# Optimization experiments

Hardware: AMD Instinct MI355X
Metric: run time of the kernel (lower is better)

The kernel has to match this reference:

```python
import jax, jax.numpy as jnp
import numpy as np

# static config (matches init_kwargs / input_specs)
LENS = (2048, 1024, 512, 256)   # per-level temporal lengths, sum = 3840
N, LQ, D_MODEL = 8, 2048, 256
M, L, P = 8, 4, 4               # heads, levels, points
D_HEAD = D_MODEL // M           # 32


def setup_inputs() -> dict:
    key = jax.random.key(0)
    ks = jax.random.split(key, 8)
    s = 0.02  # xavier-ish scale for 256-wide linears
    return {
        "query": jax.random.normal(ks[0], (N, LQ, D_MODEL), jnp.float32),
        "reference_points": jax.random.uniform(ks[1], (N, LQ, L, 1), dtype=jnp.float32),
        "input_flatten": jax.random.normal(ks[2], (N, sum(LENS), D_MODEL), jnp.float32),
        "input_temporal_lens": jnp.array(LENS, jnp.int32),
        "input_level_start_index": jnp.array(np.concatenate([[0], np.cumsum(LENS)[:-1]]), jnp.int32),
        "W_val": jax.random.normal(ks[3], (D_MODEL, D_MODEL), jnp.float32) * s,
        "b_val": jnp.zeros((D_MODEL,), jnp.float32),
        "W_off": jax.random.normal(ks[4], (M * L * P, D_MODEL), jnp.float32) * s,
        "b_off": jax.random.normal(ks[5], (M * L * P,), jnp.float32),  # mimics linspace bias init
        "W_attn": jax.random.normal(ks[6], (M * L * P, D_MODEL), jnp.float32) * s,
        "b_attn": jnp.zeros((M * L * P,), jnp.float32),
    }


def _sample_level(v, x, T):
    """1D bilinear sampling with zero padding, matching F.grid_sample
    (mode='bilinear', padding_mode='zeros', align_corners=False) on a (1,T) map.
    v: (N, T, M, D) level values; x: (N, Lq, M, P) normalized locations in [0,1].
    Returns (N, Lq, M, P, D)."""
    n, lq, m, p = x.shape
    ix = x * T - 0.5
    ix0 = jnp.floor(ix)
    w1 = (ix - ix0)[..., None]            # (N,Lq,M,P,1)
    i0 = ix0.astype(jnp.int32)

    def gather(idx):
        valid = ((idx >= 0) & (idx < T)).astype(v.dtype)
        idxc = jnp.clip(idx, 0, T - 1)
        flat = idxc.transpose(0, 1, 3, 2).reshape(n, lq * p, m)       # (N, Lq*P, M)
        g = jnp.take_along_axis(v, flat[..., None], axis=1)           # (N, Lq*P, M, D)
        g = g * valid.transpose(0, 1, 3, 2).reshape(n, lq * p, m)[..., None]
        return g.reshape(n, lq, p, m, -1).transpose(0, 1, 3, 2, 4)    # (N,Lq,M,P,D)

    return gather(i0) * (1.0 - w1) + gather(i0 + 1) * w1


def _deform_core(value, lens, loc, attn):
    """value: (N, S, M, D); loc: (N,Lq,M,L,P,1); attn: (N,Lq,M,L,P) -> (N,Lq,M*D)"""
    out = 0.0
    start = 0
    for lid, T in enumerate(lens):
        v = value[:, start:start + T]
        start += T
        s = _sample_level(v, loc[:, :, :, lid, :, 0], T)              # (N,Lq,M,P,D)
        out = out + jnp.einsum('nqmpd,nqmp->nqmd', s, attn[:, :, :, lid])
    n, lq, m, d = out.shape
    return out.reshape(n, lq, m * d)


def reference(query, reference_points, input_flatten, input_temporal_lens,
              input_level_start_index, W_val, b_val, W_off, b_off, W_attn, b_attn):
    lens = LENS  # static per-level lengths (needed for static slicing)
    value = (input_flatten @ W_val.T + b_val).reshape(N, sum(lens), M, D_HEAD)
    offs = (query @ W_off.T + b_off).reshape(N, LQ, M, L, P, 1)
    attn = jax.nn.softmax((query @ W_attn.T + b_attn).reshape(N, LQ, M, L * P), axis=-1)
    attn = attn.reshape(N, LQ, M, L, P)
    # reference_points last dim == 1, offset_normalizer=None branch
    norm = jnp.asarray(lens, query.dtype)[None, None, None, :, None, None]
    loc = reference_points[:, :, None, :, None, :] + offs / norm      # (N,Lq,M,L,P,1)
    # fp32 path of the torch module returns the core output WITHOUT output_proj
    return _deform_core(value, lens, loc, attn)
```

## Files before the change

kernel.cpp:

```cpp
#include <hip/hip_runtime.h>
#include <cstddef>

namespace {

constexpr int NB    = 8;
constexpr int LQn   = 2048;
constexpr int DM    = 256;
constexpr int S_TOT = 3840;

typedef __attribute__((ext_vector_type(8))) short  short8;
typedef __attribute__((ext_vector_type(4))) float  f32x4;
typedef __attribute__((ext_vector_type(8))) _Float16 half8;
typedef __attribute__((ext_vector_type(2))) _Float16 half2v;

__device__ inline unsigned short f2bf(float f) {
  union { float f; unsigned u; } v; v.f = f;
  const unsigned u = v.u;
  return (unsigned short)((u + 0x7FFFu + ((u >> 16) & 1u)) >> 16);
}

__global__ __launch_bounds__(256) void gemm_bf16_k(
    const float* __restrict__ A,
    const float* __restrict__ Wa, const float* __restrict__ ba,
    const float* __restrict__ Wb, const float* __restrict__ bb,
    _Float16* __restrict__ out)
{
  __shared__ short As[128 * 64];
  __shared__ short Bs[128 * 64];

  const int tid  = threadIdx.x;
  const int lane = tid & 63;
  const int wid  = tid >> 6;
  const int wm   = wid >> 1;
  const int wn   = wid & 1;
  const int r0   = blockIdx.x * 128;
  const int c0   = blockIdx.y * 128;

  const float* W    = Wa;
  const float* bias = ba;
  int cw0 = c0;
  if (Wb != nullptr && c0 >= 128) { W = Wb; bias = bb; cw0 = c0 - 128; }

  f32x4 acc[4][4] = {};

  float bv[4];
  #pragma unroll
  for (int ni = 0; ni < 4; ++ni)
    bv[ni] = bias[cw0 + wn * 64 + ni * 16 + (lane & 15)];

  f32x4 pa0[4], pa1[4], pw0[4], pw1[4];

  auto load_tiles = [&](int k0) {
    #pragma unroll
    for (int i = 0; i < 4; ++i) {
      const int ch  = tid + i * 256;
      const int row = ch >> 3;
      const int kg  = ch & 7;
      const size_t goff = (size_t)(r0 + row) * DM + k0 + kg * 8;
      pa0[i] = *reinterpret_cast<const f32x4*>(&A[goff]);
      pa1[i] = *reinterpret_cast<const f32x4*>(&A[goff + 4]);
      const size_t woff = (size_t)(cw0 + row) * DM + k0 + kg * 8;
      pw0[i] = *reinterpret_cast<const f32x4*>(&W[woff]);
      pw1[i] = *reinterpret_cast<const f32x4*>(&W[woff + 4]);
    }
  };

  load_tiles(0);

  for (int k = 0; k < 4; ++k) {
    #pragma unroll
    for (int i = 0; i < 4; ++i) {
      const int ch  = tid + i * 256;
      const int row = ch >> 3;
      const int kg  = ch & 7;
      short8 sa, sw;
      #pragma unroll
      for (int j = 0; j < 4; ++j) {
        sa[j]     = (short)f2bf(pa0[i][j]);
        sa[j + 4] = (short)f2bf(pa1[i][j]);
        sw[j]     = (short)f2bf(pw0[i][j]);
        sw[j + 4] = (short)f2bf(pw1[i][j]);
      }
      const int byte = row * 128 + ((kg * 16) ^ ((row & 7) << 4));
      *reinterpret_cast<short8*>(reinterpret_cast<char*>(As) + byte) = sa;
      *reinterpret_cast<short8*>(reinterpret_cast<char*>(Bs) + byte) = sw;
    }
    if (k < 3) load_tiles((k + 1) * 64);

    asm volatile("s_waitcnt lgkmcnt(0)" ::: "memory");
    __builtin_amdgcn_sched_barrier(0);
    __builtin_amdgcn_s_barrier();
    __builtin_amdgcn_sched_barrier(0);

    #pragma unroll
    for (int ks = 0; ks < 2; ++ks) {
      const int kb = (ks * 32 + (lane >> 4) * 8) * 2;
      short8 af[4], bf[4];
      #pragma unroll
      for (int mi = 0; mi < 4; ++mi) {
        const int row = wm * 64 + mi * 16 + (lane & 15);
        const int byte = row * 128 + (kb ^ ((row & 7) << 4));
        af[mi] = *reinterpret_cast<const short8*>(
            reinterpret_cast<const char*>(As) + byte);
      }
      #pragma unroll
      for (int ni = 0; ni < 4; ++ni) {
        const int col = wn * 64 + ni * 16 + (lane & 15);
        const int byte = col * 128 + (kb ^ ((col & 7) << 4));
        bf[ni] = *reinterpret_cast<const short8*>(
            reinterpret_cast<const char*>(Bs) + byte);
      }
      #pragma unroll
      for (int mi = 0; mi < 4; ++mi)
        #pragma unroll
        for (int ni = 0; ni < 4; ++ni)
          acc[mi][ni] = __builtin_amdgcn_mfma_f32_16x16x32_bf16(
              af[mi], bf[ni], acc[mi][ni], 0, 0, 0);
    }

    asm volatile("s_waitcnt lgkmcnt(0)" ::: "memory");
    __builtin_amdgcn_sched_barrier(0);
    __builtin_amdgcn_s_barrier();
    __builtin_amdgcn_sched_barrier(0);
  }

  #pragma unroll
  for (int mi = 0; mi < 4; ++mi) {
    const int row = r0 + wm * 64 + mi * 16 + (lane >> 4) * 4;
    #pragma unroll
    for (int ni = 0; ni < 4; ++ni) {
      const int col = c0 + wn * 64 + ni * 16 + (lane & 15);
      #pragma unroll
      for (int j = 0; j < 4; ++j)
        out[(size_t)(row + j) * DM + col] = (_Float16)(acc[mi][ni][j] + bv[ni]);
    }
  }
}

__global__ __launch_bounds__(256) void sample_k(
    const _Float16* __restrict__ proj,
    const float* __restrict__ refp,
    const _Float16* __restrict__ value,
    float* __restrict__ out)
{
  constexpr int QPB = 8;
  __shared__ _Float16 proj_s[QPB][256];
  __shared__ float    ref_s[QPB][4];
  __shared__ uint4    tap_s[QPB][8 * 17];

  const int d     = blockIdx.x;
  const int n     = d & 7;
  const int chunk = d >> 3;
  const int row0q = n * LQn + chunk * QPB;
  const int t     = threadIdx.x;

  reinterpret_cast<half8*>(&proj_s[0][0])[t] =
      reinterpret_cast<const half8*>(proj + (size_t)row0q * DM)[t];
  if (t < QPB * 4)
    reinterpret_cast<float*>(ref_s)[t] = refp[(size_t)row0q * 4 + t];
  __syncthreads();

  const int   lens[4]   = {2048, 1024, 512, 256};
  const int   starts[4] = {0, 2048, 3072, 3584};

  {
    const int q   = t >> 5;
    const int m   = (t >> 2) & 7;
    const int sub = t & 3;
    const int j0  = m * 16 + sub * 4;

    float lg[4], off[4];
    #pragma unroll
    for (int i = 0; i < 4; ++i) {
      lg[i]  = (float)proj_s[q][128 + j0 + i];
      off[i] = (float)proj_s[q][j0 + i];
    }
    float mx = fmaxf(fmaxf(lg[0], lg[1]), fmaxf(lg[2], lg[3]));
    mx = fmaxf(mx, __shfl_xor(mx, 1));
    mx = fmaxf(mx, __shfl_xor(mx, 2));
    float e[4], s = 0.f;
    #pragma unroll
    for (int i = 0; i < 4; ++i) { e[i] = __expf(lg[i] - mx); s += e[i]; }
    s += __shfl_xor(s, 1);
    s += __shfl_xor(s, 2);
    const float inv = 1.f / s;

    const int   T  = lens[sub];
    const int   st = starts[sub];
    const float fT = (float)T;
    const float rf = ref_s[q][sub];
    #pragma unroll
    for (int i = 0; i < 4; ++i) {
      const float a  = e[i] * inv;
      const float ix = fmaf(rf, fT, off[i] - 0.5f);
      const float fl = floorf(ix);
      const float w1 = ix - fl;
      const int   i0 = (int)fl;
      const int   i1 = i0 + 1;
      const float wa = (i0 >= 0 && i0 < T) ? a * (1.f - w1) : 0.f;
      const float wb = (i1 >= 0 && i1 < T) ? a * w1 : 0.f;
      const int   r0b = (st + min(max(i0, 0), T - 1)) * 512;
      const int   r1b = (st + min(max(i1, 0), T - 1)) * 512;
      union { half2v h; unsigned u; } pw;
      pw.h.x = (_Float16)wa; pw.h.y = (_Float16)wb;
      uint4 ent; ent.x = pw.u; ent.y = (unsigned)r0b; ent.z = (unsigned)r1b; ent.w = 0u;
      tap_s[q][m * 17 + sub * 4 + i] = ent;
    }
  }
  __syncthreads();

  const int q  = t >> 5;
  const int m  = (t >> 2) & 7;
  const int dg = t & 3;
  const char* vb = reinterpret_cast<const char*>(value) +
                   (size_t)n * S_TOT * 512 + m * 64 + dg * 16;

  float acc[8] = {};
  #pragma unroll
  for (int tap = 0; tap < 16; ++tap) {
    const uint4 e = tap_s[q][m * 17 + tap];
    union { unsigned u; half2v h; } pw; pw.u = e.x;
    const float wa = (float)pw.h.x;
    const float wb = (float)pw.h.y;
    const half8 v0 = *reinterpret_cast<const half8*>(vb + e.y);
    const half8 v1 = *reinterpret_cast<const half8*>(vb + e.z);
    #pragma unroll
    for (int j = 0; j < 8; ++j)
      acc[j] = fmaf(wa, (float)v0[j], fmaf(wb, (float)v1[j], acc[j]));
  }

  float* op = &out[(size_t)(row0q + q) * DM + m * 32 + dg * 8];
  f32x4 o0 = {acc[0], acc[1], acc[2], acc[3]};
  f32x4 o1 = {acc[4], acc[5], acc[6], acc[7]};
  *reinterpret_cast<f32x4*>(op)     = o0;
  *reinterpret_cast<f32x4*>(op + 4) = o1;
}

}

extern "C" void kernel_launch(void* const* d_in, const int* in_sizes, int n_in,
                              void* d_out, int out_size, void* d_ws, size_t ws_size,
                              hipStream_t stream) {
  const float* query  = (const float*)d_in[0];
  const float* refp   = (const float*)d_in[1];
  const float* inflat = (const float*)d_in[2];
  const float* W_val  = (const float*)d_in[5];
  const float* b_val  = (const float*)d_in[6];
  const float* W_off  = (const float*)d_in[7];
  const float* b_off  = (const float*)d_in[8];
  const float* W_attn = (const float*)d_in[9];
  const float* b_attn = (const float*)d_in[10];
  float* out = (float*)d_out;

  _Float16* value_h = (_Float16*)d_ws;
  _Float16* proj_h  = (_Float16*)((char*)d_ws +
                      (size_t)NB * S_TOT * DM * sizeof(_Float16));

  dim3 blk(256);

  gemm_bf16_k<<<dim3((NB * S_TOT) / 128, DM / 128), blk, 0, stream>>>(
      inflat, W_val, b_val, nullptr, nullptr, value_h);

  gemm_bf16_k<<<dim3((NB * LQn) / 128, DM / 128), blk, 0, stream>>>(
      query, W_off, b_off, W_attn, b_attn, proj_h);

  sample_k<<<dim3(NB * LQn / 8), blk, 0, stream>>>(proj_h, refp, value_h, out);
}
```

Before: 46.67 us.

## Merge both projection GEMMs into one launch and split sampling taps across threads

The value and query projection GEMMs now run as one grid of 736 blocks, with each block picking its operands from its block index. This removes a launch and lets the two GEMMs fill the GPU together. The sampling kernel now uses 512 threads, and each (query, head, dgroup) is split across two threads that each handle 8 of the 16 taps, combined with a shuffle. This doubles the memory-level parallelism for the gathers. The shared-memory staging of proj and refp is dropped in favour of direct loads, which cuts one barrier but adds redundant global reads.

```diff
diff --git a/kernel.cpp b/kernel.cpp
--- a/kernel.cpp
+++ b/kernel.cpp
@@ -11,6 +11,7 @@
 typedef __attribute__((ext_vector_type(8))) short  short8;
 typedef __attribute__((ext_vector_type(4))) float  f32x4;
 typedef __attribute__((ext_vector_type(8))) _Float16 half8;
+typedef __attribute__((ext_vector_type(4))) _Float16 half4;
 typedef __attribute__((ext_vector_type(2))) _Float16 half2v;
 
 __device__ inline unsigned short f2bf(float f) {
@@ -20,10 +21,11 @@
 }
 
 __global__ __launch_bounds__(256) void gemm_bf16_k(
-    const float* __restrict__ A,
-    const float* __restrict__ Wa, const float* __restrict__ ba,
-    const float* __restrict__ Wb, const float* __restrict__ bb,
-    _Float16* __restrict__ out)
+    const float* __restrict__ A_val, const float* __restrict__ A_prj,
+    const float* __restrict__ W_val, const float* __restrict__ b_val,
+    const float* __restrict__ W_off, const float* __restrict__ b_off,
+    const float* __restrict__ W_att, const float* __restrict__ b_att,
+    _Float16* __restrict__ out_val, _Float16* __restrict__ out_prj)
 {
   __shared__ short As[128 * 64];
   __shared__ short Bs[128 * 64];
@@ -33,20 +35,27 @@
   const int wid  = tid >> 6;
   const int wm   = wid >> 1;
   const int wn   = wid & 1;
-  const int r0   = blockIdx.x * 128;
-  const int c0   = blockIdx.y * 128;
-
-  const float* W    = Wa;
-  const float* bias = ba;
-  int cw0 = c0;
-  if (Wb != nullptr && c0 >= 128) { W = Wb; bias = bb; cw0 = c0 - 128; }
+
+  const int id = blockIdx.x;
+  const float *A, *W, *bias;
+  _Float16* out;
+  int r0, c0;
+  if (id < 480) {
+    const int rb = id >> 1, c = id & 1;
+    A = A_val; out = out_val; r0 = rb * 128; c0 = c * 128;
+    W = W_val + (size_t)c0 * DM; bias = b_val + c0;
+  } else {
+    const int j = id - 480, rb = j >> 1, c = j & 1;
+    A = A_prj; out = out_prj; r0 = rb * 128; c0 = c * 128;
+    W = c ? W_att : W_off; bias = c ? b_att : b_off;
+  }
 
   f32x4 acc[4][4] = {};
 
   float bv[4];
   #pragma unroll
   for (int ni = 0; ni < 4; ++ni)
-    bv[ni] = bias[cw0 + wn * 64 + ni * 16 + (lane & 15)];
+    bv[ni] = bias[wn * 64 + ni * 16 + (lane & 15)];
 
   f32x4 pa0[4], pa1[4], pw0[4], pw1[4];
 
@@ -59,7 +68,7 @@
       const size_t goff = (size_t)(r0 + row) * DM + k0 + kg * 8;
       pa0[i] = *reinterpret_cast<const f32x4*>(&A[goff]);
       pa1[i] = *reinterpret_cast<const f32x4*>(&A[goff + 4]);
-      const size_t woff = (size_t)(cw0 + row) * DM + k0 + kg * 8;
+      const size_t woff = (size_t)row * DM + k0 + kg * 8;
       pw0[i] = *reinterpret_cast<const f32x4*>(&W[woff]);
       pw1[i] = *reinterpret_cast<const f32x4*>(&W[woff + 4]);
     }
@@ -137,44 +146,36 @@
   }
 }
 
-__global__ __launch_bounds__(256) void sample_k(
+__global__ __launch_bounds__(512) void sample_k(
     const _Float16* __restrict__ proj,
     const float* __restrict__ refp,
     const _Float16* __restrict__ value,
     float* __restrict__ out)
 {
-  constexpr int QPB = 8;
-  __shared__ _Float16 proj_s[QPB][256];
-  __shared__ float    ref_s[QPB][4];
-  __shared__ uint4    tap_s[QPB][8 * 17];
+  __shared__ uint4 tap_s[8][136];
 
   const int d     = blockIdx.x;
   const int n     = d & 7;
   const int chunk = d >> 3;
-  const int row0q = n * LQn + chunk * QPB;
+  const int row0q = n * LQn + chunk * 8;
   const int t     = threadIdx.x;
 
-  reinterpret_cast<half8*>(&proj_s[0][0])[t] =
-      reinterpret_cast<const half8*>(proj + (size_t)row0q * DM)[t];
-  if (t < QPB * 4)
-    reinterpret_cast<float*>(ref_s)[t] = refp[(size_t)row0q * 4 + t];
-  __syncthreads();
-
-  const int   lens[4]   = {2048, 1024, 512, 256};
-  const int   starts[4] = {0, 2048, 3072, 3584};
-
-  {
+  const int lens[4]   = {2048, 1024, 512, 256};
+  const int starts[4] = {0, 2048, 3072, 3584};
+
+  if (t < 256) {
     const int q   = t >> 5;
     const int m   = (t >> 2) & 7;
     const int sub = t & 3;
     const int j0  = m * 16 + sub * 4;
-
+    const size_t prow = (size_t)(row0q + q) * DM;
+
+    const half4 offv = *reinterpret_cast<const half4*>(&proj[prow + j0]);
+    const half4 lgv  = *reinterpret_cast<const half4*>(&proj[prow + 128 + j0]);
     float lg[4], off[4];
     #pragma unroll
-    for (int i = 0; i < 4; ++i) {
-      lg[i]  = (float)proj_s[q][128 + j0 + i];
-      off[i] = (float)proj_s[q][j0 + i];
-    }
+    for (int i = 0; i < 4; ++i) { lg[i] = (float)lgv[i]; off[i] = (float)offv[i]; }
+
     float mx = fmaxf(fmaxf(lg[0], lg[1]), fmaxf(lg[2], lg[3]));
     mx = fmaxf(mx, __shfl_xor(mx, 1));
     mx = fmaxf(mx, __shfl_xor(mx, 2));
@@ -188,7 +189,7 @@
     const int   T  = lens[sub];
     const int   st = starts[sub];
     const float fT = (float)T;
-    const float rf = ref_s[q][sub];
+    const float rf = refp[(size_t)(row0q + q) * 4 + sub];
     #pragma unroll
     for (int i = 0; i < 4; ++i) {
       const float a  = e[i] * inv;
@@ -209,16 +210,18 @@
   }
   __syncthreads();
 
-  const int q  = t >> 5;
-  const int m  = (t >> 2) & 7;
-  const int dg = t & 3;
+  const int q  = t >> 6;
+  const int l  = t & 63;
+  const int m  = l >> 3;
+  const int dg = l & 3;
+  const int th = (l >> 2) & 1;
   const char* vb = reinterpret_cast<const char*>(value) +
                    (size_t)n * S_TOT * 512 + m * 64 + dg * 16;
 
   float acc[8] = {};
   #pragma unroll
-  for (int tap = 0; tap < 16; ++tap) {
-    const uint4 e = tap_s[q][m * 17 + tap];
+  for (int i = 0; i < 8; ++i) {
+    const uint4 e = tap_s[q][m * 17 + th * 8 + i];
     union { unsigned u; half2v h; } pw; pw.u = e.x;
     const float wa = (float)pw.h.x;
     const float wb = (float)pw.h.y;
@@ -229,11 +232,16 @@
       acc[j] = fmaf(wa, (float)v0[j], fmaf(wb, (float)v1[j], acc[j]));
   }
 
-  float* op = &out[(size_t)(row0q + q) * DM + m * 32 + dg * 8];
-  f32x4 o0 = {acc[0], acc[1], acc[2], acc[3]};
-  f32x4 o1 = {acc[4], acc[5], acc[6], acc[7]};
-  *reinterpret_cast<f32x4*>(op)     = o0;
-  *reinterpret_cast<f32x4*>(op + 4) = o1;
+  #pragma unroll
+  for (int j = 0; j < 8; ++j) acc[j] += __shfl_xor(acc[j], 4);
+
+  if (th == 0) {
+    float* op = &out[(size_t)(row0q + q) * DM + m * 32 + dg * 8];
+    f32x4 o0 = {acc[0], acc[1], acc[2], acc[3]};
+    f32x4 o1 = {acc[4], acc[5], acc[6], acc[7]};
+    *reinterpret_cast<f32x4*>(op)     = o0;
+    *reinterpret_cast<f32x4*>(op + 4) = o1;
+  }
 }
 
 }
@@ -256,13 +264,10 @@
   _Float16* proj_h  = (_Float16*)((char*)d_ws +
                       (size_t)NB * S_TOT * DM * sizeof(_Float16));
 
-  dim3 blk(256);
-
-  gemm_bf16_k<<<dim3((NB * S_TOT) / 128, DM / 128), blk, 0, stream>>>(
-      inflat, W_val, b_val, nullptr, nullptr, value_h);
-
-  gemm_bf16_k<<<dim3((NB * LQn) / 128, DM / 128), blk, 0, stream>>>(
-      query, W_off, b_off, W_attn, b_attn, proj_h);
-
-  sample_k<<<dim3(NB * LQn / 8), blk, 0, stream>>>(proj_h, refp, value_h, out);
-}
+  gemm_bf16_k<<<dim3(736), dim3(256), 0, stream>>>(
+      inflat, query, W_val, b_val, W_off, b_off, W_attn, b_attn,
+      value_h, proj_h);
+
+  sample_k<<<dim3(NB * LQn / 8), dim3(512), 0, stream>>>(
+      proj_h, refp, value_h, out);
+}
```

Result: faster. 43.93 us (-5.9%).
